# Optimization experiments

Hardware: AMD Instinct MI355X
Metric: run time of the kernel (lower is better)

## Reference

```python
import jax, jax.numpy as jnp
import numpy as np

NUM_COUNT = 256  # hard-coded in feature_select


def setup_inputs() -> dict:
    key = jax.random.key(0)
    k1, k2 = jax.random.split(key)
    B, H, S, D = 16, 16, 577, 1024
    hidden_states = jax.random.normal(k1, (B, S, D), dtype=jnp.float32)
    attention = jax.random.uniform(k2, (B, H, S, S), dtype=jnp.float32)
    return {"hidden_states": hidden_states, "attention": attention}


def _select_indices(attention):
    """Vectorized equivalent of the per-batch/per-head python set-union loop.

    For each head (in order), add exactly per_head_num new patch indices taken
    in decreasing CLS-attention order, skipping indices already in the set.
    Index 0 (CLS) is always included. Returns sorted indices [B, NUM_COUNT+1].
    """
    B, H, S, _ = attention.shape
    p = NUM_COUNT // H  # per_head_num
    cls_attn = attention[:, :, 0, :]  # [B, H, S] : CLS row of each head
    member = jnp.zeros((B, S), dtype=bool).at[:, 0].set(True)  # {0} always in set
    b_idx = jnp.arange(B)[:, None]
    for h in range(H):  # H=16 structurally-distinct sequential steps
        a = cls_attn[:, h, 1:]  # [B, S-1], patches only (index 0 excluded)
        ranked = jnp.argsort(-a, axis=-1) + 1  # descending order, indices in [1, S)
        is_new = ~member[b_idx, ranked]  # [B, S-1]
        take = is_new & (jnp.cumsum(is_new.astype(jnp.int32), axis=-1) <= p)
        # ranked is a permutation per row -> scatter-set is safe
        add = jnp.zeros((B, S), dtype=bool).at[b_idx, ranked].set(take)
        member = member | add
    n_sel = NUM_COUNT + 1  # exactly 257 members per batch by construction
    S_range = jnp.arange(S)[None, :]
    idx = jnp.sort(jnp.where(member, S_range, S), axis=-1)[:, :n_sel]  # ascending
    return idx


def reference(hidden_states, attention):
    idx = _select_indices(attention)  # [B, 257]
    selected_query = jnp.take_along_axis(hidden_states, idx[:, :, None], axis=1)
    return hidden_states, selected_query
```

## Files before the change

### kernel.cpp

```cpp
#include <hip/hip_runtime.h>
#include <float.h>

#define NB 16
#define NH 16
#define SS 577
#define DD 1024
#define NSEL 257
#define TOPK 64
#define PH 16

#define HIDDEN_ELEMS (NB * SS * DD)
#define HIDDEN_V4 (HIDDEN_ELEMS / 4)
#define SEL_ELEMS (NB * NSEL * DD)
#define SEL_V4 (SEL_ELEMS / 4)

__device__ __forceinline__ void pair_max_reduce(float& bv, int& bi) {
    #pragma unroll
    for (int off = 1; off < 64; off <<= 1) {
        float ov = __shfl_xor(bv, off, 64);
        int   oi = __shfl_xor(bi, off, 64);
        if (ov > bv || (ov == bv && oi < bi)) { bv = ov; bi = oi; }
    }
}

__global__ __launch_bounds__(256)
void k_topk_copy(const float* __restrict__ hidden,
                 const float* __restrict__ attn,
                 float* __restrict__ out,
                 int* __restrict__ cand) {
    int blk = blockIdx.x;
    if (blk < NB * NH) {
        if (threadIdx.x >= 64) return;
        int lane = threadIdx.x;
        const float* row = attn + (size_t)blk * ((size_t)SS * SS);
        float v[9];
        #pragma unroll
        for (int s = 0; s < 9; ++s) v[s] = row[1 + lane + 64 * s];

        float bv; int bi;
        bv = -FLT_MAX; bi = 0x7fffffff;
        #pragma unroll
        for (int s = 0; s < 9; ++s)
            if (v[s] > bv) { bv = v[s]; bi = 1 + lane + 64 * s; }

        int mine = 0;
        for (int t = 0; t < TOPK; ++t) {
            float wv = bv; int wi = bi;
            pair_max_reduce(wv, wi);
            if (lane == t) mine = wi;
            int wl = (wi - 1) & 63;
            if (lane == wl) {
                int wslot = (wi - 1) >> 6;
                #pragma unroll
                for (int s = 0; s < 9; ++s) if (s == wslot) v[s] = -FLT_MAX;
                bv = -FLT_MAX; bi = 0x7fffffff;
                #pragma unroll
                for (int s = 0; s < 9; ++s)
                    if (v[s] > bv) { bv = v[s]; bi = 1 + lane + 64 * s; }
            }
        }
        cand[blk * TOPK + lane] = mine;
    } else {
        const float4* src = (const float4*)hidden;
        float4* dst = (float4*)out;
        size_t stride = (size_t)(gridDim.x - NB * NH) * blockDim.x;
        for (size_t i = (size_t)(blk - NB * NH) * blockDim.x + threadIdx.x;
             i < (size_t)HIDDEN_V4; i += stride)
            dst[i] = src[i];
    }
}

__global__ __launch_bounds__(64)
void k_merge(const float* __restrict__ attn,
             const int* __restrict__ cand,
             int* __restrict__ sel) {
    int b = blockIdx.x;
    int lane = threadIdx.x;
    __shared__ unsigned char member[SS];
    for (int i = lane; i < SS; i += 64) member[i] = 0;
    if (lane == 0) member[0] = 1;
    __builtin_amdgcn_wave_barrier();

    unsigned long long lowmask = (lane == 0) ? 0ull : ((1ull << lane) - 1ull);

    for (int h = 0; h < NH; ++h) {
        int c = cand[(b * NH + h) * TOPK + lane];
        int avail = member[c] ? 0 : 1;
        unsigned long long bal = __ballot(avail);
        int rank = __popcll(bal & lowmask);
        if (avail && rank < PH) member[c] = 1;
        int got = __popcll(bal);
        if (got < PH) {
            int need = (got > PH ? 0 : PH - got);
            const float* row = attn + (size_t)(b * NH + h) * ((size_t)SS * SS);
            float v[9];
            #pragma unroll
            for (int s = 0; s < 9; ++s) {
                int idx = 1 + lane + 64 * s;
                v[s] = member[idx] ? -FLT_MAX : row[idx];
            }
            for (int t = 0; t < need; ++t) {
                float bv = -FLT_MAX; int bi = 0x7fffffff;
                #pragma unroll
                for (int s = 0; s < 9; ++s)
                    if (v[s] > bv) { bv = v[s]; bi = 1 + lane + 64 * s; }
                pair_max_reduce(bv, bi);
                int wl = (bi - 1) & 63;
                if (lane == wl) {
                    int wslot = (bi - 1) >> 6;
                    #pragma unroll
                    for (int s = 0; s < 9; ++s) if (s == wslot) v[s] = -FLT_MAX;
                    member[bi] = 1;
                }
                __builtin_amdgcn_wave_barrier();
            }
        }
        __builtin_amdgcn_wave_barrier();
    }

    int pos = 0;
    #pragma unroll
    for (int s = 0; s < 10; ++s) {
        int i = s * 64 + lane;
        int m = (i < SS) ? (member[i] ? 1 : 0) : 0;
        unsigned long long bal = __ballot(m);
        int rank = __popcll(bal & lowmask);
        if (m) sel[b * NSEL + pos + rank] = i;
        pos += __popcll(bal);
    }
}

__global__ __launch_bounds__(256)
void k_gather(const float* __restrict__ hidden,
              const int* __restrict__ sel,
              float* __restrict__ out) {
    const float4* src = (const float4*)hidden;
    float4* dst = (float4*)(out + (size_t)HIDDEN_ELEMS);
    size_t stride = (size_t)gridDim.x * blockDim.x;
    for (size_t i = (size_t)blockIdx.x * blockDim.x + threadIdx.x;
         i < (size_t)SEL_V4; i += stride) {
        size_t rowi = i >> 8;
        int d4 = (int)(i & 255);
        int b = (int)(rowi / NSEL);
        int j = (int)(rowi - (size_t)b * NSEL);
        int r = sel[b * NSEL + j];
        dst[i] = src[(((size_t)(b * SS + r)) << 8) + d4];
    }
}

extern "C" void kernel_launch(void* const* d_in, const int* in_sizes, int n_in,
                              void* d_out, int out_size, void* d_ws, size_t ws_size,
                              hipStream_t stream) {
    const float* hidden = (const float*)d_in[0];
    const float* attn   = (const float*)d_in[1];
    float* out = (float*)d_out;
    int* cand = (int*)d_ws;
    int* sel  = cand + NB * NH * TOPK;

    k_topk_copy<<<NB * NH + 1792, 256, 0, stream>>>(hidden, attn, out, cand);
    k_merge<<<NB, 64, 0, stream>>>(attn, cand, sel);
    k_gather<<<1024, 256, 0, stream>>>(hidden, sel, out);
}
```

Baseline: 438.7 us.

## Fuse merge into top-k kernel via last-block atomic counter; nontemporal stores

The separate per-batch merge kernel is folded into the top-k/copy kernel. The last head block of each batch finishes, detected with a threadfence and an atomic counter, and performs the set-union merge and index compaction. This removes one kernel launch and its dependency gap. It adds a memset of the counters, and the copy and gather stores now use nontemporal hints to avoid polluting cache.

```diff
diff --git a/kernel.cpp b/kernel.cpp
--- a/kernel.cpp
+++ b/kernel.cpp
@@ -13,6 +13,9 @@
 #define HIDDEN_V4 (HIDDEN_ELEMS / 4)
 #define SEL_ELEMS (NB * NSEL * DD)
 #define SEL_V4 (SEL_ELEMS / 4)
+#define NCOPY 1792
+
+using f32x4 = __attribute__((ext_vector_type(4))) float;
 
 __device__ __forceinline__ void pair_max_reduce(float& bv, int& bi) {
     #pragma unroll
@@ -24,21 +27,25 @@
 }
 
 __global__ __launch_bounds__(256)
-void k_topk_copy(const float* __restrict__ hidden,
-                 const float* __restrict__ attn,
-                 float* __restrict__ out,
-                 int* __restrict__ cand) {
+void k_sel_copy(const float* __restrict__ hidden,
+                const float* __restrict__ attn,
+                float* __restrict__ out,
+                int* __restrict__ cand,
+                int* __restrict__ sel,
+                unsigned int* __restrict__ cnt) {
     int blk = blockIdx.x;
     if (blk < NB * NH) {
         if (threadIdx.x >= 64) return;
         int lane = threadIdx.x;
+        int b = blk >> 4;
+        unsigned long long lowmask = (lane == 0) ? 0ull : ((1ull << lane) - 1ull);
+
         const float* row = attn + (size_t)blk * ((size_t)SS * SS);
         float v[9];
         #pragma unroll
         for (int s = 0; s < 9; ++s) v[s] = row[1 + lane + 64 * s];
 
-        float bv; int bi;
-        bv = -FLT_MAX; bi = 0x7fffffff;
+        float bv = -FLT_MAX; int bi = 0x7fffffff;
         #pragma unroll
         for (int s = 0; s < 9; ++s)
             if (v[s] > bv) { bv = v[s]; bi = 1 + lane + 64 * s; }
@@ -60,73 +67,71 @@
             }
         }
         cand[blk * TOPK + lane] = mine;
+
+        __threadfence();
+        int old = 0;
+        if (lane == 0) old = (int)atomicAdd(&cnt[b], 1u);
+        old = __shfl(old, 0, 64);
+        if (old != NH - 1) return;
+        __threadfence();
+
+        __shared__ unsigned char member[SS];
+        for (int i = lane; i < SS; i += 64) member[i] = 0;
+        if (lane == 0) member[0] = 1;
+        __builtin_amdgcn_wave_barrier();
+
+        for (int h = 0; h < NH; ++h) {
+            int c = cand[(b * NH + h) * TOPK + lane];
+            int avail = member[c] ? 0 : 1;
+            unsigned long long bal = __ballot(avail);
+            int rank = __popcll(bal & lowmask);
+            if (avail && rank < PH) member[c] = 1;
+            int got = __popcll(bal);
+            if (got < PH) {
+                int need = PH - got;
+                const float* hrow = attn + (size_t)(b * NH + h) * ((size_t)SS * SS);
+                float w[9];
+                #pragma unroll
+                for (int s = 0; s < 9; ++s) {
+                    int idx = 1 + lane + 64 * s;
+                    w[s] = member[idx] ? -FLT_MAX : hrow[idx];
+                }
+                for (int t = 0; t < need; ++t) {
+                    float fv = -FLT_MAX; int fi = 0x7fffffff;
+                    #pragma unroll
+                    for (int s = 0; s < 9; ++s)
+                        if (w[s] > fv) { fv = w[s]; fi = 1 + lane + 64 * s; }
+                    pair_max_reduce(fv, fi);
+                    int wl = (fi - 1) & 63;
+                    if (lane == wl) {
+                        int wslot = (fi - 1) >> 6;
+                        #pragma unroll
+                        for (int s = 0; s < 9; ++s) if (s == wslot) w[s] = -FLT_MAX;
+                        member[fi] = 1;
+                    }
+                    __builtin_amdgcn_wave_barrier();
+                }
+            }
+            __builtin_amdgcn_wave_barrier();
+        }
+
+        int pos = 0;
+        #pragma unroll
+        for (int s = 0; s < 10; ++s) {
+            int i = s * 64 + lane;
+            int m = (i < SS) ? (member[i] ? 1 : 0) : 0;
+            unsigned long long bal = __ballot(m);
+            int rank = __popcll(bal & lowmask);
+            if (m) sel[b * NSEL + pos + rank] = i;
+            pos += __popcll(bal);
+        }
     } else {
-        const float4* src = (const float4*)hidden;
-        float4* dst = (float4*)out;
-        size_t stride = (size_t)(gridDim.x - NB * NH) * blockDim.x;
+        const f32x4* src = (const f32x4*)hidden;
+        f32x4* dst = (f32x4*)out;
+        size_t stride = (size_t)NCOPY * blockDim.x;
         for (size_t i = (size_t)(blk - NB * NH) * blockDim.x + threadIdx.x;
              i < (size_t)HIDDEN_V4; i += stride)
-            dst[i] = src[i];
-    }
-}
-
-__global__ __launch_bounds__(64)
-void k_merge(const float* __restrict__ attn,
-             const int* __restrict__ cand,
-             int* __restrict__ sel) {
-    int b = blockIdx.x;
-    int lane = threadIdx.x;
-    __shared__ unsigned char member[SS];
-    for (int i = lane; i < SS; i += 64) member[i] = 0;
-    if (lane == 0) member[0] = 1;
-    __builtin_amdgcn_wave_barrier();
-
-    unsigned long long lowmask = (lane == 0) ? 0ull : ((1ull << lane) - 1ull);
-
-    for (int h = 0; h < NH; ++h) {
-        int c = cand[(b * NH + h) * TOPK + lane];
-        int avail = member[c] ? 0 : 1;
-        unsigned long long bal = __ballot(avail);
-        int rank = __popcll(bal & lowmask);
-        if (avail && rank < PH) member[c] = 1;
-        int got = __popcll(bal);
-        if (got < PH) {
-            int need = (got > PH ? 0 : PH - got);
-            const float* row = attn + (size_t)(b * NH + h) * ((size_t)SS * SS);
-            float v[9];
-            #pragma unroll
-            for (int s = 0; s < 9; ++s) {
-                int idx = 1 + lane + 64 * s;
-                v[s] = member[idx] ? -FLT_MAX : row[idx];
-            }
-            for (int t = 0; t < need; ++t) {
-                float bv = -FLT_MAX; int bi = 0x7fffffff;
-                #pragma unroll
-                for (int s = 0; s < 9; ++s)
-                    if (v[s] > bv) { bv = v[s]; bi = 1 + lane + 64 * s; }
-                pair_max_reduce(bv, bi);
-                int wl = (bi - 1) & 63;
-                if (lane == wl) {
-                    int wslot = (bi - 1) >> 6;
-                    #pragma unroll
-                    for (int s = 0; s < 9; ++s) if (s == wslot) v[s] = -FLT_MAX;
-                    member[bi] = 1;
-                }
-                __builtin_amdgcn_wave_barrier();
-            }
-        }
-        __builtin_amdgcn_wave_barrier();
-    }
-
-    int pos = 0;
-    #pragma unroll
-    for (int s = 0; s < 10; ++s) {
-        int i = s * 64 + lane;
-        int m = (i < SS) ? (member[i] ? 1 : 0) : 0;
-        unsigned long long bal = __ballot(m);
-        int rank = __popcll(bal & lowmask);
-        if (m) sel[b * NSEL + pos + rank] = i;
-        pos += __popcll(bal);
+            __builtin_nontemporal_store(src[i], &dst[i]);
     }
 }
 
@@ -134,8 +139,8 @@
 void k_gather(const float* __restrict__ hidden,
               const int* __restrict__ sel,
               float* __restrict__ out) {
-    const float4* src = (const float4*)hidden;
-    float4* dst = (float4*)(out + (size_t)HIDDEN_ELEMS);
+    const f32x4* src = (const f32x4*)hidden;
+    f32x4* dst = (f32x4*)(out + (size_t)HIDDEN_ELEMS);
     size_t stride = (size_t)gridDim.x * blockDim.x;
     for (size_t i = (size_t)blockIdx.x * blockDim.x + threadIdx.x;
          i < (size_t)SEL_V4; i += stride) {
@@ -144,7 +149,7 @@
         int b = (int)(rowi / NSEL);
         int j = (int)(rowi - (size_t)b * NSEL);
         int r = sel[b * NSEL + j];
-        dst[i] = src[(((size_t)(b * SS + r)) << 8) + d4];
+        __builtin_nontemporal_store(src[(((size_t)(b * SS + r)) << 8) + d4], &dst[i]);
     }
 }
 
@@ -156,8 +161,9 @@
     float* out = (float*)d_out;
     int* cand = (int*)d_ws;
     int* sel  = cand + NB * NH * TOPK;
+    unsigned int* cnt = (unsigned int*)(sel + NB * NSEL);
 
-    k_topk_copy<<<NB * NH + 1792, 256, 0, stream>>>(hidden, attn, out, cand);
-    k_merge<<<NB, 64, 0, stream>>>(attn, cand, sel);
+    hipMemsetAsync(cnt, 0, NB * sizeof(unsigned int), stream);
+    k_sel_copy<<<NB * NH + NCOPY, 256, 0, stream>>>(hidden, attn, out, cand, sel, cnt);
     k_gather<<<1024, 256, 0, stream>>>(hidden, sel, out);
 }
```

Measured after the change: 443.7 us. Within noise of the previous version (+1.1%).
